# Kernel tuning notes

Measured on AMD Instinct MI355X. Metric: run time of the kernel, lower is better.

The kernel has to match this reference:

```python
import jax, jax.numpy as jnp
import numpy as np


def setup_inputs() -> dict:
    key = jax.random.key(0)
    # x: node features (N, C); only N is used by the module's math.
    x = jax.random.normal(key, (8192, 2048), dtype=jnp.float32)
    return {"x": x}


def reference(x):
    N = x.shape[0]
    M = N + 4
    # adj = eye(N+4); adj[N:, N:] = 1.0 (bottom-right 4x4 block of ones)
    A = jnp.eye(M, dtype=jnp.float32)
    A = A.at[N:, N:].set(1.0)
    # gen_adj: D = diag(rowsum(A)^-0.5); out = (A @ D).T @ D = D * A.T * D
    # Expressed as O(M^2) row/column scaling (algebraically identical to the
    # original diag-matmul formulation, avoiding the O(M^3) dense matmuls).
    d = jnp.sum(A, axis=1) ** -0.5  # (M,)
    adj = (d[:, None] * A.T) * d[None, :]
    return adj
```

## Files before the change

### kernel.cpp

```cpp
#include <hip/hip_runtime.h>
#include <math.h>


__global__ void ADJ_fixup_kernel(float* __restrict__ out, int N, int M) {
    int i = blockIdx.x * blockDim.x + threadIdx.x;
    if (i < N) {
        out[(size_t)i * (size_t)M + (size_t)i] = 1.0f;
    } else if (i < M) {
        size_t row_base = (size_t)i * (size_t)M;
        #pragma unroll
        for (int j = 0; j < 4; ++j) {
            out[row_base + (size_t)(N + j)] = 0.25f;
        }
    }
}

extern "C" void kernel_launch(void* const* d_in, const int* in_sizes, int n_in,
                              void* d_out, int out_size, void* d_ws, size_t ws_size,
                              hipStream_t stream) {
    (void)d_in; (void)in_sizes; (void)n_in; (void)d_ws; (void)ws_size;

    int M = (int)(sqrt((double)out_size) + 0.5);
    int N = M - 4;

    float* out = (float*)d_out;

    hipMemsetAsync(d_out, 0, (size_t)out_size * sizeof(float), stream);

    int block = 256;
    int grid = (M + block - 1) / block;
    ADJ_fixup_kernel<<<grid, block, 0, stream>>>(out, N, M);
}
```

Baseline: 286.4 us.

## Fuse memset and diagonal fixup into a single vectorized row-fill kernel

```diff
diff --git a/kernel.cpp b/kernel.cpp
--- a/kernel.cpp
+++ b/kernel.cpp
@@ -2,15 +2,27 @@
 #include <math.h>
 
 
-__global__ void ADJ_fixup_kernel(float* __restrict__ out, int N, int M) {
-    int i = blockIdx.x * blockDim.x + threadIdx.x;
-    if (i < N) {
-        out[(size_t)i * (size_t)M + (size_t)i] = 1.0f;
-    } else if (i < M) {
-        size_t row_base = (size_t)i * (size_t)M;
-        #pragma unroll
-        for (int j = 0; j < 4; ++j) {
-            out[row_base + (size_t)(N + j)] = 0.25f;
+__global__ __launch_bounds__(256) void adj_fill_kernel(float4* __restrict__ out,
+                                                       int N, int M4) {
+    const int row = blockIdx.x;
+    const size_t base = (size_t)row * (size_t)M4;
+
+    if (row < N) {
+        const int dc   = row >> 2;
+        const int lane = row & 3;
+        for (int c = threadIdx.x; c < M4; c += blockDim.x) {
+            float4 v = make_float4(0.f, 0.f, 0.f, 0.f);
+            if (c == dc) {
+                ((float*)&v)[lane] = 1.0f;
+            }
+            out[base + c] = v;
+        }
+    } else {
+        const int last = M4 - 1;
+        for (int c = threadIdx.x; c < M4; c += blockDim.x) {
+            float4 v = (c == last) ? make_float4(0.25f, 0.25f, 0.25f, 0.25f)
+                                   : make_float4(0.f, 0.f, 0.f, 0.f);
+            out[base + c] = v;
         }
     }
 }
@@ -22,12 +34,7 @@
 
     int M = (int)(sqrt((double)out_size) + 0.5);
     int N = M - 4;
+    int M4 = M >> 2;
 
-    float* out = (float*)d_out;
-
-    hipMemsetAsync(d_out, 0, (size_t)out_size * sizeof(float), stream);
-
-    int block = 256;
-    int grid = (M + block - 1) / block;
-    ADJ_fixup_kernel<<<grid, block, 0, stream>>>(out, N, M);
+    adj_fill_kernel<<<M, 256, 0, stream>>>((float4*)d_out, N, M4);
 }
```

After: 309.9 us. 1.08x slower.
